# Kernel optimization log

Hardware: AMD Instinct MI355X
Metric: run time of the kernel (lower is better)

Reference implementation:

```python
import jax, jax.numpy as jnp
import numpy as np

B, CH, H, W = 128, 3, 224, 224
R = 14
S = R * R  # 196 superpixels
DIMS = [11, 96, 192, 384, 768, 768]
BN_EPS = 1e-5


def setup_inputs() -> dict:
    key = jax.random.key(0)
    ks = jax.random.split(key, 64)
    inp = {}
    inp["x"] = jax.random.normal(ks[0], (B, CH, H, W), jnp.float32)
    inp["sliced"] = jax.random.randint(ks[1], (B, H, W), 0, S, jnp.int32)
    ki = 2
    for i in range(5):
        ci, co = DIMS[i], DIMS[i + 1]
        inp[f"w{i}"] = jax.random.normal(ks[ki], (co, ci), jnp.float32) / np.sqrt(ci); ki += 1
        inp[f"b{i}"] = jnp.zeros((co,), jnp.float32)
        inp[f"g{i}"] = jnp.ones((co,), jnp.float32)
        inp[f"be{i}"] = jnp.zeros((co,), jnp.float32)
        inp[f"rm{i}"] = jax.random.normal(ks[ki], (co,), jnp.float32) * 0.1; ki += 1
        inp[f"rv{i}"] = jax.random.uniform(ks[ki], (co,), jnp.float32) + 0.5; ki += 1
    return inp


def _seg_features(x, sliced):
    # x: [B,3,H,W] float, sliced: [B,H,W] int labels in [0,S)
    b, c, h, w = x.shape
    n = h * w
    ids = sliced.reshape(b, n).astype(jnp.int32)
    gid = (jnp.arange(b, dtype=jnp.int32)[:, None] * S + ids).reshape(-1)  # [B*N]

    counts = jax.ops.segment_sum(jnp.ones((b * n,), x.dtype), gid, num_segments=b * S)  # [B*S]
    rows = jnp.repeat(jnp.arange(h, dtype=x.dtype), w)
    cols = jnp.tile(jnp.arange(w, dtype=x.dtype), h)
    coords = jnp.stack([rows, cols], -1)                       # [N,2]
    coords_b = jnp.broadcast_to(coords, (b, n, 2)).reshape(b * n, 2)
    coord_sum = jax.ops.segment_sum(coords_b, gid, num_segments=b * S)  # [B*S,2]

    rgb = x.reshape(b, c, n).transpose(0, 2, 1).reshape(b * n, c)       # [B*N,3]
    rgb_sum = jax.ops.segment_sum(rgb, gid, num_segments=b * S)
    rgb_sq = jax.ops.segment_sum(rgb * rgb, gid, num_segments=b * S)

    cnt = counts[:, None]
    safe = jnp.maximum(cnt, 1.0)
    mean_coord = coord_sum / safe                              # [B*S,2]
    mean_rgb = rgb_sum / safe                                  # [B*S,3]
    # torch .std is unbiased; NaN (count<=1) replaced by 0
    var = (rgb_sq - cnt * mean_rgb * mean_rgb) / jnp.maximum(cnt - 1.0, 1.0)
    std = jnp.where(cnt > 1.0, jnp.sqrt(jnp.maximum(var, 0.0)), 0.0)

    mc = mean_coord.reshape(b, S, 2)
    mr = mean_rgb.reshape(b, S, 3)
    sd = std.reshape(b, S, 3)
    # gather pixel at the (truncated) mean location of each segment
    ri = jnp.clip(mc[..., 0].astype(jnp.int32), 0, h - 1)      # [B,S]
    ci = jnp.clip(mc[..., 1].astype(jnp.int32), 0, w - 1)
    gathered = x[jnp.arange(b)[:, None], :, ri, ci]            # [B,S,3]

    feat = jnp.concatenate([mc, mr, sd, gathered], -1)         # [B,S,11]
    feat = feat * (counts.reshape(b, S, 1) > 0).astype(x.dtype)  # absent segments stay 0
    return feat.transpose(0, 2, 1).reshape(b, 11, R, R)


def _conv_bn(h, w, b, g, be, rm, rv, act):
    # 1x1 conv == channel contraction
    h = jnp.einsum('bchw,oc->bohw', h, w) + b[None, :, None, None]
    scale = g / jnp.sqrt(rv + BN_EPS)
    h = (h - rm[None, :, None, None]) * scale[None, :, None, None] + be[None, :, None, None]
    return jax.nn.relu(h) if act else h


def reference(x, sliced,
              w0, b0, g0, be0, rm0, rv0,
              w1, b1, g1, be1, rm1, rv1,
              w2, b2, g2, be2, rm2, rv2,
              w3, b3, g3, be3, rm3, rv3,
              w4, b4, g4, be4, rm4, rv4):
    params = [(w0, b0, g0, be0, rm0, rv0), (w1, b1, g1, be1, rm1, rv1),
              (w2, b2, g2, be2, rm2, rv2), (w3, b3, g3, be3, rm3, rv3),
              (w4, b4, g4, be4, rm4, rv4)]
    h = _seg_features(x, sliced)                # [B,11,14,14]
    for i, (w, b, g, be, rm, rv) in enumerate(params):
        h = _conv_bn(h, w, b, g, be, rm, rv, act=(i < 4))  # last block: BN only
    return (sliced, h)
```

## Files before the change

### kernel.cpp

```cpp
#include <hip/hip_runtime.h>
#include <hip/hip_bf16.h>

#define HW    50176
#define IMGW  224
#define SEG   196
#define NBATCH 128
#define NCOL  (NBATCH * SEG)
#define PB    14
#define CHUNK (HW / PB)
#define VCHUNK (CHUNK / 4)

typedef __attribute__((ext_vector_type(8))) short bf16x8;
typedef __attribute__((ext_vector_type(4))) float f32x4;
typedef unsigned long long u64;

static __device__ __forceinline__ ushort f2bf(float v) {
    __hip_bfloat16 h = __float2bfloat16(v);
    return *reinterpret_cast<ushort*>(&h);
}

__global__ __launch_bounds__(256) void seg_accum(const float* __restrict__ x,
                                                 const int*   __restrict__ sl,
                                                 float*       __restrict__ stats) {
    __shared__ u64 ls[4][SEG];
    int b    = blockIdx.x / PB;
    int part = blockIdx.x % PB;
    int tid  = threadIdx.x;

    for (int i = tid; i < 4 * SEG; i += 256) (&ls[0][0])[i] = 0ull;
    __syncthreads();

    const float* xb = x + (size_t)b * 3 * HW;
    const int*   sb = sl + (size_t)b * HW;
    int v0 = part * VCHUNK;

    for (int vi = tid; vi < VCHUNK; vi += 256) {
        int vg = v0 + vi;
        int4   id4 = ((const int4*)sb)[vg];
        float4 r4  = ((const float4*)xb)[vg];
        float4 g4  = ((const float4*)(xb + HW))[vg];
        float4 b4  = ((const float4*)(xb + 2 * HW))[vg];
        int p   = vg * 4;
        int row = p / IMGW;
        int col = p - row * IMGW;
        u64 rowbits = ((u64)1 << 48) | ((u64)(unsigned)row << 24);

#pragma unroll
        for (int q = 0; q < 4; ++q) {
            int   id = (q == 0) ? id4.x : (q == 1) ? id4.y : (q == 2) ? id4.z : id4.w;
            float r  = (q == 0) ? r4.x  : (q == 1) ? r4.y  : (q == 2) ? r4.z  : r4.w;
            float g  = (q == 0) ? g4.x  : (q == 1) ? g4.y  : (q == 2) ? g4.z  : g4.w;
            float bl = (q == 0) ? b4.x  : (q == 1) ? b4.y  : (q == 2) ? b4.z  : b4.w;

            unsigned qr  = (unsigned)fmaf(r,  8192.f, 131072.5f);
            unsigned qg  = (unsigned)fmaf(g,  8192.f, 131072.5f);
            unsigned qb  = (unsigned)fmaf(bl, 8192.f, 131072.5f);
            unsigned qr2 = (unsigned)fmaf(r * r,  2048.f, 0.5f);
            unsigned qg2 = (unsigned)fmaf(g * g,  2048.f, 0.5f);
            unsigned qb2 = (unsigned)fmaf(bl * bl, 2048.f, 0.5f);

            atomicAdd(&ls[0][id], rowbits | (unsigned)(col + q));
            atomicAdd(&ls[1][id], ((u64)qg  << 32) | qr);
            atomicAdd(&ls[2][id], ((u64)qr2 << 32) | qb);
            atomicAdd(&ls[3][id], ((u64)qb2 << 32) | qg2);
        }
    }
    __syncthreads();

    const float inv_s = 1.f / 8192.f, inv_q = 1.f / 2048.f;
    for (int i = tid; i < SEG; i += 256) {
        u64 v0p = ls[0][i];
        unsigned cnt = (unsigned)(v0p >> 48);
        if (!cnt) continue;
        float fc   = (float)cnt;
        float rows = (float)((unsigned)(v0p >> 24) & 0xFFFFFFu);
        float cols = (float)((unsigned)v0p & 0xFFFFFFu);
        u64 v1 = ls[1][i], v2 = ls[2][i], v3 = ls[3][i];
        float bias = 16.f * fc;
        float rsum = (float)(unsigned)v1         * inv_s - bias;
        float gsum = (float)(unsigned)(v1 >> 32) * inv_s - bias;
        float bsum = (float)(unsigned)v2         * inv_s - bias;
        float rsq  = (float)(unsigned)(v2 >> 32) * inv_q;
        float gsq  = (float)(unsigned)v3         * inv_q;
        float bsq  = (float)(unsigned)(v3 >> 32) * inv_q;

        size_t base = (size_t)b * SEG + i;
        atomicAdd(&stats[0 * NCOL + base], fc);
        atomicAdd(&stats[1 * NCOL + base], rows);
        atomicAdd(&stats[2 * NCOL + base], cols);
        atomicAdd(&stats[3 * NCOL + base], rsum);
        atomicAdd(&stats[4 * NCOL + base], gsum);
        atomicAdd(&stats[5 * NCOL + base], bsum);
        atomicAdd(&stats[6 * NCOL + base], rsq);
        atomicAdd(&stats[7 * NCOL + base], gsq);
        atomicAdd(&stats[8 * NCOL + base], bsq);
    }
}

__global__ __launch_bounds__(256) void feat_build(const float* __restrict__ x,
                                                  const float* __restrict__ stats,
                                                  ushort*      __restrict__ F) {
    int n = blockIdx.x * 256 + threadIdx.x;
    if (n >= NCOL) return;
    int b = n / SEG;

    float cnt  = stats[n];
    float safe = fmaxf(cnt, 1.f);
    float inv  = 1.f / safe;
    float mrow = stats[1 * NCOL + n] * inv;
    float mcol = stats[2 * NCOL + n] * inv;
    float mr   = stats[3 * NCOL + n] * inv;
    float mg   = stats[4 * NCOL + n] * inv;
    float mb   = stats[5 * NCOL + n] * inv;
    float den  = fmaxf(cnt - 1.f, 1.f);
    float vr = (stats[6 * NCOL + n] - cnt * mr * mr) / den;
    float vg = (stats[7 * NCOL + n] - cnt * mg * mg) / den;
    float vb = (stats[8 * NCOL + n] - cnt * mb * mb) / den;
    bool  has2 = cnt > 1.f;
    float sr = has2 ? sqrtf(fmaxf(vr, 0.f)) : 0.f;
    float sg = has2 ? sqrtf(fmaxf(vg, 0.f)) : 0.f;
    float sb = has2 ? sqrtf(fmaxf(vb, 0.f)) : 0.f;

    int ri = min(max((int)mrow, 0), IMGW - 1);
    int ci = min(max((int)mcol, 0), IMGW - 1);
    const float* xb = x + (size_t)b * 3 * HW;
    int pi = ri * IMGW + ci;
    float gr = xb[pi], gg = xb[HW + pi], gb = xb[2 * HW + pi];

    float mask = cnt > 0.f ? 1.f : 0.f;
    ushort* Fr = F + (size_t)n * 64;
#pragma unroll
    for (int k = 11; k < 64; ++k) Fr[k] = 0;
    Fr[0]  = f2bf(mrow * mask);
    Fr[1]  = f2bf(mcol * mask);
    Fr[2]  = f2bf(mr * mask);
    Fr[3]  = f2bf(mg * mask);
    Fr[4]  = f2bf(mb * mask);
    Fr[5]  = f2bf(sr * mask);
    Fr[6]  = f2bf(sg * mask);
    Fr[7]  = f2bf(sb * mask);
    Fr[8]  = f2bf(gr * mask);
    Fr[9]  = f2bf(gg * mask);
    Fr[10] = f2bf(gb * mask);
}

__global__ __launch_bounds__(256) void convert_w(const float* __restrict__ src,
                                                 ushort* __restrict__ dst,
                                                 int Cout, int K, int Kpad, int total) {
    int i = blockIdx.x * 256 + threadIdx.x;
    if (i >= total) return;
    int o = i / Kpad, k = i - o * Kpad;
    float v = (o < Cout && k < K) ? src[(size_t)o * K + k] : 0.f;
    dst[i] = f2bf(v);
}

__global__ __launch_bounds__(256) void gemm_mfma(const ushort* __restrict__ Aact,
                                                 const ushort* __restrict__ Wb,
                                                 void* __restrict__ outp,
                                                 const float* __restrict__ bias,
                                                 const float* __restrict__ gam,
                                                 const float* __restrict__ bet,
                                                 const float* __restrict__ rm,
                                                 const float* __restrict__ rv,
                                                 int Kpad, int Cout, int OutStride,
                                                 int act, int final_out) {
    __shared__ ushort As[2][128 * 64];
    __shared__ ushort Bs[2][128 * 64];

    int tid  = threadIdx.x;
    int lane = tid & 63;
    int wid  = tid >> 6;
    int wm   = wid & 1;
    int wn   = wid >> 1;

    int nbx  = gridDim.x, nby = gridDim.y;
    int nwg  = nbx * nby;
    int orig = blockIdx.y * nbx + blockIdx.x;
    int xcd  = orig & 7;
    int q    = nwg >> 3, r = nwg & 7;
    int wgid = (xcd < r ? xcd * (q + 1) : r * (q + 1) + (xcd - r) * q) + (orig >> 3);
    int bx   = wgid / nby;
    int by   = wgid - bx * nby;
    int n0   = bx * 128;
    int o0   = by * 128;

    int mrow = lane & 15;
    int quad = lane >> 4;
    int swz  = mrow & 7;

    f32x4 acc[4][4];
#pragma unroll
    for (int i = 0; i < 4; ++i)
#pragma unroll
        for (int j = 0; j < 4; ++j) acc[i][j] = (f32x4){0.f, 0.f, 0.f, 0.f};

    const ushort* aSrc[4];
    const ushort* bSrc[4];
    int ldsDst[4];
#pragma unroll
    for (int p = 0; p < 4; ++p) {
        int flat = p * 256 + tid;
        int row  = flat >> 3, kg = flat & 7;
        int kgs  = kg ^ (row & 7);
        aSrc[p]  = Aact + (size_t)(n0 + row) * Kpad + kgs * 8;
        bSrc[p]  = Wb   + (size_t)(o0 + row) * Kpad + kgs * 8;
        ldsDst[p] = (p * 256 + wid * 64) * 8;
    }

    auto stage = [&](int buf, int kt) {
        int kb = kt * 64;
#pragma unroll
        for (int p = 0; p < 4; ++p)
            __builtin_amdgcn_global_load_lds(
                (const __attribute__((address_space(1))) void*)(aSrc[p] + kb),
                (__attribute__((address_space(3))) void*)(&As[buf][ldsDst[p]]),
                16, 0, 0);
#pragma unroll
        for (int p = 0; p < 4; ++p)
            __builtin_amdgcn_global_load_lds(
                (const __attribute__((address_space(1))) void*)(bSrc[p] + kb),
                (__attribute__((address_space(3))) void*)(&Bs[buf][ldsDst[p]]),
                16, 0, 0);
    };

    auto compute = [&](int buf) {
#pragma unroll
        for (int ks = 0; ks < 2; ++ks) {
            bf16x8 af[4], bfr[4];
            int gbase = ks * 4 + quad;
            int slot  = (gbase ^ swz) * 8;
#pragma unroll
            for (int i = 0; i < 4; ++i)
                af[i] = *(const bf16x8*)&As[buf][(size_t)(wm * 64 + i * 16 + mrow) * 64 + slot];
#pragma unroll
            for (int j = 0; j < 4; ++j)
                bfr[j] = *(const bf16x8*)&Bs[buf][(size_t)(wn * 64 + j * 16 + mrow) * 64 + slot];
#pragma unroll
            for (int i = 0; i < 4; ++i)
#pragma unroll
                for (int j = 0; j < 4; ++j)
                    acc[i][j] = __builtin_amdgcn_mfma_f32_16x16x32_bf16(af[i], bfr[j], acc[i][j], 0, 0, 0);
        }
    };

    int ktiles = Kpad >> 6;

    stage(0, 0);
    asm volatile("s_waitcnt vmcnt(0)" ::: "memory");
    __builtin_amdgcn_s_barrier();

    int cur = 0;
    for (int t = 0; t < ktiles - 1; ++t) {
        stage(cur ^ 1, t + 1);
        compute(cur);
        asm volatile("s_waitcnt vmcnt(0)" ::: "memory");
        __builtin_amdgcn_s_barrier();
        cur ^= 1;
    }
    compute(cur);

#pragma unroll
    for (int j = 0; j < 4; ++j) {
        int o = o0 + wn * 64 + j * 16 + mrow;
        float al = 0.f, bt = 0.f;
        if (o < Cout) {
            float sc = gam[o] / sqrtf(rv[o] + 1e-5f);
            al = sc;
            bt = (bias[o] - rm[o]) * sc + bet[o];
        }
#pragma unroll
        for (int i = 0; i < 4; ++i) {
            int nbase = n0 + wm * 64 + i * 16 + quad * 4;
#pragma unroll
            for (int rr = 0; rr < 4; ++rr) {
                float v = acc[i][j][rr] * al + bt;
                if (act) v = fmaxf(v, 0.f);
                int n = nbase + rr;
                if (final_out) {
                    int b = n / SEG, s = n - b * SEG;
                    ((float*)outp)[(size_t)b * 768 * SEG + (size_t)o * SEG + s] = v;
                } else {
                    ((ushort*)outp)[(size_t)n * OutStride + o] = f2bf(v);
                }
            }
        }
    }
}

__global__ __launch_bounds__(256) void copy_sliced(const int4* __restrict__ sl,
                                                   float4* __restrict__ out) {
    int i = blockIdx.x * 256 + threadIdx.x;
    int4 v = sl[i];
    out[i] = make_float4((float)v.x, (float)v.y, (float)v.z, (float)v.w);
}

extern "C" void kernel_launch(void* const* d_in, const int* in_sizes, int n_in,
                              void* d_out, int out_size, void* d_ws, size_t ws_size,
                              hipStream_t stream) {
    const float* x  = (const float*)d_in[0];
    const int*   sl = (const int*)d_in[1];
    const float* Wp[5], *Bp[5], *Gp[5], *BEp[5], *RMp[5], *RVp[5];
    for (int i = 0; i < 5; ++i) {
        Wp[i]  = (const float*)d_in[2 + 6 * i + 0];
        Bp[i]  = (const float*)d_in[2 + 6 * i + 1];
        Gp[i]  = (const float*)d_in[2 + 6 * i + 2];
        BEp[i] = (const float*)d_in[2 + 6 * i + 3];
        RMp[i] = (const float*)d_in[2 + 6 * i + 4];
        RVp[i] = (const float*)d_in[2 + 6 * i + 5];
    }
    float* out = (float*)d_out;

    const int Kpad[5]  = {64, 128, 256, 384, 768};
    const int Kreal[5] = {11, 96, 192, 384, 768};
    const int Cout[5]  = {96, 192, 384, 768, 768};
    const int Opad[5]  = {128, 256, 384, 768, 768};

    char* wsb = (char*)d_ws;
    float*  stats = (float*)wsb;
    wsb += (size_t)9 * NCOL * sizeof(float);
    ushort* F = (ushort*)wsb;
    wsb += (size_t)NCOL * 64 * sizeof(ushort);
    ushort* Wpad[5];
    for (int i = 0; i < 5; ++i) {
        Wpad[i] = (ushort*)wsb;
        wsb += (size_t)Opad[i] * Kpad[i] * sizeof(ushort);
    }
    ushort* bufA = (ushort*)wsb;
    wsb += (size_t)NCOL * 384 * sizeof(ushort);
    ushort* bufB = (ushort*)wsb;

    hipMemsetAsync(stats, 0, (size_t)9 * NCOL * sizeof(float), stream);

    for (int i = 0; i < 5; ++i) {
        int total = Opad[i] * Kpad[i];
        convert_w<<<(total + 255) / 256, 256, 0, stream>>>(
            Wp[i], Wpad[i], Cout[i], Kreal[i], Kpad[i], total);
    }

    seg_accum<<<NBATCH * PB, 256, 0, stream>>>(x, sl, stats);
    feat_build<<<(NCOL + 255) / 256, 256, 0, stream>>>(x, stats, F);

    const int NT = NCOL / 128;
    gemm_mfma<<<dim3(NT, Opad[0] / 128), 256, 0, stream>>>(
        F, Wpad[0], bufA, Bp[0], Gp[0], BEp[0], RMp[0], RVp[0],
        Kpad[0], Cout[0], Opad[0], 1, 0);
    gemm_mfma<<<dim3(NT, Opad[1] / 128), 256, 0, stream>>>(
        bufA, Wpad[1], bufB, Bp[1], Gp[1], BEp[1], RMp[1], RVp[1],
        Kpad[1], Cout[1], Opad[1], 1, 0);
    gemm_mfma<<<dim3(NT, Opad[2] / 128), 256, 0, stream>>>(
        bufB, Wpad[2], bufA, Bp[2], Gp[2], BEp[2], RMp[2], RVp[2],
        Kpad[2], Cout[2], Opad[2], 1, 0);
    gemm_mfma<<<dim3(NT, Opad[3] / 128), 256, 0, stream>>>(
        bufA, Wpad[3], bufB, Bp[3], Gp[3], BEp[3], RMp[3], RVp[3],
        Kpad[3], Cout[3], Opad[3], 1, 0);
    gemm_mfma<<<dim3(NT, Opad[4] / 128), 256, 0, stream>>>(
        bufB, Wpad[4], out + (size_t)NBATCH * HW, Bp[4], Gp[4], BEp[4], RMp[4], RVp[4],
        Kpad[4], Cout[4], 0, 0, 1);

    copy_sliced<<<(NBATCH * HW / 4) / 256, 256, 0, stream>>>((const int4*)sl,
                                                             (float4*)out);
}
```

Measured before the change: 413.1 us.

## Fuse feature build and first three conv layers into one LDS-resident kernel

Replaces the feat_build kernel and the first three gemm launches with a single kernel. Each 64-column tile builds its 11-feature rows in shared memory, then runs layers 0-2 with activations kept in swizzled LDS, streaming double-buffered weight tiles through global_load_lds. Only the 384-channel layer-2 output goes to global memory. This removes the global round trips of the F matrix and the intermediate activations, plus two launches. The BN scale/shift computation in gemm_mfma is also moved before the main loop. In exchange the 64-wide tiles reload all weights per block and use a smaller per-wave MFMA tile, and the large shared-memory footprint may limit occupancy.

New measurement: 411.0 us. About the same (-0.5%).

```diff
diff --git a/kernel.cpp b/kernel.cpp
--- a/kernel.cpp
+++ b/kernel.cpp
@@ -97,53 +97,6 @@
     }
 }
 
-__global__ __launch_bounds__(256) void feat_build(const float* __restrict__ x,
-                                                  const float* __restrict__ stats,
-                                                  ushort*      __restrict__ F) {
-    int n = blockIdx.x * 256 + threadIdx.x;
-    if (n >= NCOL) return;
-    int b = n / SEG;
-
-    float cnt  = stats[n];
-    float safe = fmaxf(cnt, 1.f);
-    float inv  = 1.f / safe;
-    float mrow = stats[1 * NCOL + n] * inv;
-    float mcol = stats[2 * NCOL + n] * inv;
-    float mr   = stats[3 * NCOL + n] * inv;
-    float mg   = stats[4 * NCOL + n] * inv;
-    float mb   = stats[5 * NCOL + n] * inv;
-    float den  = fmaxf(cnt - 1.f, 1.f);
-    float vr = (stats[6 * NCOL + n] - cnt * mr * mr) / den;
-    float vg = (stats[7 * NCOL + n] - cnt * mg * mg) / den;
-    float vb = (stats[8 * NCOL + n] - cnt * mb * mb) / den;
-    bool  has2 = cnt > 1.f;
-    float sr = has2 ? sqrtf(fmaxf(vr, 0.f)) : 0.f;
-    float sg = has2 ? sqrtf(fmaxf(vg, 0.f)) : 0.f;
-    float sb = has2 ? sqrtf(fmaxf(vb, 0.f)) : 0.f;
-
-    int ri = min(max((int)mrow, 0), IMGW - 1);
-    int ci = min(max((int)mcol, 0), IMGW - 1);
-    const float* xb = x + (size_t)b * 3 * HW;
-    int pi = ri * IMGW + ci;
-    float gr = xb[pi], gg = xb[HW + pi], gb = xb[2 * HW + pi];
-
-    float mask = cnt > 0.f ? 1.f : 0.f;
-    ushort* Fr = F + (size_t)n * 64;
-#pragma unroll
-    for (int k = 11; k < 64; ++k) Fr[k] = 0;
-    Fr[0]  = f2bf(mrow * mask);
-    Fr[1]  = f2bf(mcol * mask);
-    Fr[2]  = f2bf(mr * mask);
-    Fr[3]  = f2bf(mg * mask);
-    Fr[4]  = f2bf(mb * mask);
-    Fr[5]  = f2bf(sr * mask);
-    Fr[6]  = f2bf(sg * mask);
-    Fr[7]  = f2bf(sb * mask);
-    Fr[8]  = f2bf(gr * mask);
-    Fr[9]  = f2bf(gg * mask);
-    Fr[10] = f2bf(gb * mask);
-}
-
 __global__ __launch_bounds__(256) void convert_w(const float* __restrict__ src,
                                                  ushort* __restrict__ dst,
                                                  int Cout, int K, int Kpad, int total) {
@@ -152,6 +105,184 @@
     int o = i / Kpad, k = i - o * Kpad;
     float v = (o < Cout && k < K) ? src[(size_t)o * K + k] : 0.f;
     dst[i] = f2bf(v);
+}
+
+#define SH_W   0
+#define SH_F   16384
+#define SH_A0  20480
+#define SH_A1  28672
+
+__global__ __launch_bounds__(256) void fused_l012(
+    const float* __restrict__ x,
+    const float* __restrict__ stats,
+    const ushort* __restrict__ W0g, const ushort* __restrict__ W1g, const ushort* __restrict__ W2g,
+    const float* __restrict__ bias0, const float* __restrict__ gam0, const float* __restrict__ bet0,
+    const float* __restrict__ rm0,  const float* __restrict__ rv0,
+    const float* __restrict__ bias1, const float* __restrict__ gam1, const float* __restrict__ bet1,
+    const float* __restrict__ rm1,  const float* __restrict__ rv1,
+    const float* __restrict__ bias2, const float* __restrict__ gam2, const float* __restrict__ bet2,
+    const float* __restrict__ rm2,  const float* __restrict__ rv2,
+    ushort* __restrict__ outA)
+{
+    __shared__ ushort sh[45056];
+    int tid  = threadIdx.x;
+    int lane = tid & 63;
+    int wid  = tid >> 6;
+    int mrow = lane & 15;
+    int quad = lane >> 4;
+    int n0   = blockIdx.x * 64;
+
+    if (tid < 64) {
+        int r = tid, n = n0 + r;
+        float cnt  = stats[n];
+        float safe = fmaxf(cnt, 1.f);
+        float inv  = 1.f / safe;
+        float fmrow = stats[1 * NCOL + n] * inv;
+        float fmcol = stats[2 * NCOL + n] * inv;
+        float fmr   = stats[3 * NCOL + n] * inv;
+        float fmg   = stats[4 * NCOL + n] * inv;
+        float fmb   = stats[5 * NCOL + n] * inv;
+        float den  = fmaxf(cnt - 1.f, 1.f);
+        float vr = (stats[6 * NCOL + n] - cnt * fmr * fmr) / den;
+        float vg = (stats[7 * NCOL + n] - cnt * fmg * fmg) / den;
+        float vb = (stats[8 * NCOL + n] - cnt * fmb * fmb) / den;
+        bool  has2 = cnt > 1.f;
+        float sr = has2 ? sqrtf(fmaxf(vr, 0.f)) : 0.f;
+        float sg = has2 ? sqrtf(fmaxf(vg, 0.f)) : 0.f;
+        float sb = has2 ? sqrtf(fmaxf(vb, 0.f)) : 0.f;
+        int b = n / SEG;
+        int ri = min(max((int)fmrow, 0), IMGW - 1);
+        int ci = min(max((int)fmcol, 0), IMGW - 1);
+        const float* xb = x + (size_t)b * 3 * HW;
+        int pi = ri * IMGW + ci;
+        float gr = xb[pi], gg = xb[HW + pi], gb = xb[2 * HW + pi];
+        float mask = cnt > 0.f ? 1.f : 0.f;
+
+        int rx = r & 7;
+        bf16x8 v0;
+        v0[0] = (short)f2bf(fmrow * mask);
+        v0[1] = (short)f2bf(fmcol * mask);
+        v0[2] = (short)f2bf(fmr * mask);
+        v0[3] = (short)f2bf(fmg * mask);
+        v0[4] = (short)f2bf(fmb * mask);
+        v0[5] = (short)f2bf(sr * mask);
+        v0[6] = (short)f2bf(sg * mask);
+        v0[7] = (short)f2bf(sb * mask);
+        *(bf16x8*)&sh[SH_F + r * 64 + (0 ^ rx) * 8] = v0;
+        bf16x8 v1 = (bf16x8){0,0,0,0,0,0,0,0};
+        v1[0] = (short)f2bf(gr * mask);
+        v1[1] = (short)f2bf(gg * mask);
+        v1[2] = (short)f2bf(gb * mask);
+        *(bf16x8*)&sh[SH_F + r * 64 + (1 ^ rx) * 8] = v1;
+        bf16x8 z = (bf16x8){0,0,0,0,0,0,0,0};
+        for (int g = 2; g < 8; ++g)
+            *(bf16x8*)&sh[SH_F + r * 64 + (g ^ rx) * 8] = z;
+    }
+    __syncthreads();
+
+    auto stageW = [&](int buf, int ot, int kt, const ushort* Wg, int Kl) {
+#pragma unroll
+        for (int p = 0; p < 4; ++p) {
+            int flat = p * 256 + tid;
+            int row = flat >> 3, kg = flat & 7;
+            int kgs = kg ^ (row & 7);
+            const ushort* gp = Wg + (size_t)(ot * 128 + row) * Kl + kt * 64 + kgs * 8;
+            __builtin_amdgcn_global_load_lds(
+                (const __attribute__((address_space(1))) void*)gp,
+                (__attribute__((address_space(3))) void*)&sh[SH_W + buf * 8192 + (p * 256 + wid * 64) * 8],
+                16, 0, 0);
+        }
+    };
+
+    auto run_layer = [&](const ushort* Wg, int KT, int OT, int aOff, int Win,
+                         const float* bb, const float* gg_, const float* bbe,
+                         const float* rrm, const float* rrv, int CoutL,
+                         int outOff, int Wout, int toGlobal, int Kl) {
+        stageW(0, 0, 0, Wg, Kl);
+        asm volatile("s_waitcnt vmcnt(0)" ::: "memory");
+        __builtin_amdgcn_s_barrier();
+
+        int T = OT * KT, cur = 0, ot = 0, kt = 0;
+        f32x4 acc[4][2];
+        float al[2], bt[2];
+        for (int t = 0; t < T; ++t) {
+            if (kt == 0) {
+#pragma unroll
+                for (int j = 0; j < 2; ++j) {
+                    acc[0][j] = (f32x4){0.f, 0.f, 0.f, 0.f};
+                    acc[1][j] = (f32x4){0.f, 0.f, 0.f, 0.f};
+                    acc[2][j] = (f32x4){0.f, 0.f, 0.f, 0.f};
+                    acc[3][j] = (f32x4){0.f, 0.f, 0.f, 0.f};
+                    int o = ot * 128 + wid * 32 + j * 16 + mrow;
+                    float a = 0.f, c = 0.f;
+                    if (o < CoutL) {
+                        float sc = gg_[o] / sqrtf(rrv[o] + 1e-5f);
+                        a = sc;
+                        c = (bb[o] - rrm[o]) * sc + bbe[o];
+                    }
+                    al[j] = a; bt[j] = c;
+                }
+            }
+            if (t + 1 < T) {
+                int kt2 = kt + 1, ot2 = ot;
+                if (kt2 == KT) { kt2 = 0; ot2 = ot + 1; }
+                stageW(cur ^ 1, ot2, kt2, Wg, Kl);
+            }
+#pragma unroll
+            for (int ks = 0; ks < 2; ++ks) {
+                bf16x8 af[4], bfr[2];
+                int g = kt * 8 + ks * 4 + quad;
+#pragma unroll
+                for (int i = 0; i < 4; ++i) {
+                    int row = i * 16 + mrow;
+                    int slot = (g & ~7) | ((g ^ row) & 7);
+                    af[i] = *(const bf16x8*)&sh[aOff + row * Win + slot * 8];
+                }
+#pragma unroll
+                for (int j = 0; j < 2; ++j) {
+                    int wrow = wid * 32 + j * 16 + mrow;
+                    int wslot = (ks * 4 + quad) ^ (wrow & 7);
+                    bfr[j] = *(const bf16x8*)&sh[SH_W + cur * 8192 + wrow * 64 + wslot * 8];
+                }
+#pragma unroll
+                for (int i = 0; i < 4; ++i)
+#pragma unroll
+                    for (int j = 0; j < 2; ++j)
+                        acc[i][j] = __builtin_amdgcn_mfma_f32_16x16x32_bf16(af[i], bfr[j], acc[i][j], 0, 0, 0);
+            }
+            if (t + 1 < T) {
+                asm volatile("s_waitcnt vmcnt(0)" ::: "memory");
+                __builtin_amdgcn_s_barrier();
+            }
+            if (kt == KT - 1) {
+#pragma unroll
+                for (int j = 0; j < 2; ++j) {
+                    int o = ot * 128 + wid * 32 + j * 16 + mrow;
+#pragma unroll
+                    for (int i = 0; i < 4; ++i)
+#pragma unroll
+                        for (int rr = 0; rr < 4; ++rr) {
+                            float v = fmaxf(acc[i][j][rr] * al[j] + bt[j], 0.f);
+                            int row = i * 16 + quad * 4 + rr;
+                            if (toGlobal) {
+                                outA[(size_t)(n0 + row) * 384 + o] = f2bf(v);
+                            } else {
+                                int cg = o >> 3;
+                                int slot = (cg & ~7) | ((cg ^ row) & 7);
+                                sh[outOff + row * Wout + slot * 8 + (o & 7)] = f2bf(v);
+                            }
+                        }
+                }
+                kt = 0; ++ot;
+            } else ++kt;
+            cur ^= 1;
+        }
+        __syncthreads();
+    };
+
+    run_layer(W0g, 1, 1, SH_F,  64,  bias0, gam0, bet0, rm0, rv0,  96, SH_A0, 128, 0, 64);
+    run_layer(W1g, 2, 2, SH_A0, 128, bias1, gam1, bet1, rm1, rv1, 192, SH_A1, 256, 0, 128);
+    run_layer(W2g, 4, 3, SH_A1, 256, bias2, gam2, bet2, rm2, rv2, 384, 0,     384, 1, 256);
 }
 
 __global__ __launch_bounds__(256) void gemm_mfma(const ushort* __restrict__ Aact,
@@ -188,6 +319,19 @@
     int quad = lane >> 4;
     int swz  = mrow & 7;
 
+    float al4[4], bt4[4];
+#pragma unroll
+    for (int j = 0; j < 4; ++j) {
+        int o = o0 + wn * 64 + j * 16 + mrow;
+        float a = 0.f, c = 0.f;
+        if (o < Cout) {
+            float sc = gam[o] / sqrtf(rv[o] + 1e-5f);
+            a = sc;
+            c = (bias[o] - rm[o]) * sc + bet[o];
+        }
+        al4[j] = a; bt4[j] = c;
+    }
+
     f32x4 acc[4][4];
 #pragma unroll
     for (int i = 0; i < 4; ++i)
@@ -262,18 +406,12 @@
 #pragma unroll
     for (int j = 0; j < 4; ++j) {
         int o = o0 + wn * 64 + j * 16 + mrow;
-        float al = 0.f, bt = 0.f;
-        if (o < Cout) {
-            float sc = gam[o] / sqrtf(rv[o] + 1e-5f);
-            al = sc;
-            bt = (bias[o] - rm[o]) * sc + bet[o];
-        }
 #pragma unroll
         for (int i = 0; i < 4; ++i) {
             int nbase = n0 + wm * 64 + i * 16 + quad * 4;
 #pragma unroll
             for (int rr = 0; rr < 4; ++rr) {
-                float v = acc[i][j][rr] * al + bt;
+                float v = acc[i][j][rr] * al4[j] + bt4[j];
                 if (act) v = fmaxf(v, 0.f);
                 int n = nbase + rr;
                 if (final_out) {
@@ -328,6 +466,7 @@
     ushort* bufA = (ushort*)wsb;
     wsb += (size_t)NCOL * 384 * sizeof(ushort);
     ushort* bufB = (ushort*)wsb;
+    (void)F;
 
     hipMemsetAsync(stats, 0, (size_t)9 * NCOL * sizeof(float), stream);
 
@@ -338,18 +477,15 @@
     }
 
     seg_accum<<<NBATCH * PB, 256, 0, stream>>>(x, sl, stats);
-    feat_build<<<(NCOL + 255) / 256, 256, 0, stream>>>(x, stats, F);
+
+    fused_l012<<<NCOL / 64, 256, 0, stream>>>(
+        x, stats, Wpad[0], Wpad[1], Wpad[2],
+        Bp[0], Gp[0], BEp[0], RMp[0], RVp[0],
+        Bp[1], Gp[1], BEp[1], RMp[1], RVp[1],
+        Bp[2], Gp[2], BEp[2], RMp[2], RVp[2],
+        bufA);
 
     const int NT = NCOL / 128;
-    gemm_mfma<<<dim3(NT, Opad[0] / 128), 256, 0, stream>>>(
-        F, Wpad[0], bufA, Bp[0], Gp[0], BEp[0], RMp[0], RVp[0],
-        Kpad[0], Cout[0], Opad[0], 1, 0);
-    gemm_mfma<<<dim3(NT, Opad[1] / 128), 256, 0, stream>>>(
-        bufA, Wpad[1], bufB, Bp[1], Gp[1], BEp[1], RMp[1], RVp[1],
-        Kpad[1], Cout[1], Opad[1], 1, 0);
-    gemm_mfma<<<dim3(NT, Opad[2] / 128), 256, 0, stream>>>(
-        bufB, Wpad[2], bufA, Bp[2], Gp[2], BEp[2], RMp[2], RVp[2],
-        Kpad[2], Cout[2], Opad[2], 1, 0);
     gemm_mfma<<<dim3(NT, Opad[3] / 128), 256, 0, stream>>>(
         bufA, Wpad[3], bufB, Bp[3], Gp[3], BEp[3], RMp[3], RVp[3],
         Kpad[3], Cout[3], Opad[3], 1, 0);
```
